# Kernel optimization log

Hardware: AMD Instinct MI355X
Metric: run time of the kernel (lower is better)

The kernel has to match this reference:

```python
import jax, jax.numpy as jnp
import numpy as np

D = 768
Y_DIM = 3
Z_DIM = 5
LN_EPS = 1e-5
COS_EPS = 1e-8  # F.cosine_similarity eps


def setup_inputs() -> dict:
    key = jax.random.key(0)
    ks = jax.random.split(key, 12)
    B, L = 64, 512
    s = 1.0 / np.sqrt(D)
    return {
        "embeddings": jax.random.normal(ks[0], (B, L, D), jnp.float32),
        "W1": jax.random.normal(ks[1], (D, D), jnp.float32) * s,
        "b1": jnp.zeros((D,), jnp.float32),
        "W2": jax.random.normal(ks[2], (D, D), jnp.float32) * s,
        "b2": jnp.zeros((D,), jnp.float32),
        "gamma": jnp.ones((D,), jnp.float32),
        "beta": jnp.zeros((D,), jnp.float32),
        "Wy": jax.random.normal(ks[3], (D, Y_DIM), jnp.float32) * s,
        "by": jnp.zeros((Y_DIM,), jnp.float32),
        "Wz": jax.random.normal(ks[4], (D, Z_DIM), jnp.float32) * s,
        "bz": jnp.zeros((Z_DIM,), jnp.float32),
    }


def _attention_cal(data):
    # data: [B, L, D]. Original: pairwise cosine similarity [B,L,L], sum over j, /L,
    # anti_sigmoid = 1/(1+exp(x)), softmax over L.
    # Algebraic rewrite: sum_j cos(x_i, x_j) = n_i . (sum_j n_j) with n = x/||x||.
    L = data.shape[1]
    norm = jnp.linalg.norm(data, axis=-1, keepdims=True)
    n = data / jnp.maximum(norm, COS_EPS)              # [B, L, D]
    s = n.sum(axis=1)                                  # [B, D]
    attention_weight = jnp.einsum("bld,bd->bl", n, s) / L  # [B, L]
    anti_sig = 1.0 / (1.0 + jnp.exp(attention_weight))
    return jax.nn.softmax(anti_sig, axis=-1)           # [B, L]


def reference(embeddings, W1, b1, W2, b2, gamma, beta, Wy, by, Wz, bz):
    h1 = embeddings @ W1 + b1
    h2 = jax.nn.relu(h1) @ W2 + b2
    x = embeddings + h2
    mean = x.mean(axis=-1, keepdims=True)
    var = x.var(axis=-1, keepdims=True)
    ff = gamma * (x - mean) * jax.lax.rsqrt(var + LN_EPS) + beta  # [B, L, D]
    out1 = ff @ Wy + by  # [B, L, Y_DIM]
    out2 = ff @ Wz + bz  # [B, L, Z_DIM]
    return (out1, out2, _attention_cal(ff))
```

## Files before the change

kernel.cpp:

```cpp
#include <hip/hip_runtime.h>
#include <hip/hip_bf16.h>
#include <math.h>

#define D_DIM 768
#define B_DIM 64
#define L_DIM 512
#define M_DIM (B_DIM * L_DIM)
#define YD 3
#define ZD 5
#define NCAT 16
#define LN_EPS 1e-5f
#define COS_EPS 1e-8f

typedef short short8v __attribute__((ext_vector_type(8)));
typedef float f32x4  __attribute__((ext_vector_type(4)));

__device__ __forceinline__ unsigned short f2bf(float f) {
    unsigned u = __builtin_bit_cast(unsigned, f);
    u = (u + 0x7fffu + ((u >> 16) & 1u)) >> 16;
    return (unsigned short)u;
}
__device__ __forceinline__ float bf2f(unsigned short h) {
    unsigned u = ((unsigned)h) << 16;
    return __builtin_bit_cast(float, u);
}
__device__ __forceinline__ void split2(float v, unsigned short& h, unsigned short& l) {
    h = f2bf(v);
    l = f2bf(v - bf2f(h));
}

__device__ __forceinline__ void gld16(const void* g, void* l) {
    __builtin_amdgcn_global_load_lds(
        (const __attribute__((address_space(1))) void*)g,
        (__attribute__((address_space(3))) void*)l, 16, 0, 0);
}

__global__ __launch_bounds__(256)
void tsplit_kernel(const float* __restrict__ W1, const float* __restrict__ W2,
                   unsigned short* __restrict__ t1hi, unsigned short* __restrict__ t1lo,
                   unsigned short* __restrict__ t2hi, unsigned short* __restrict__ t2lo)
{
    const float* W = blockIdx.z ? W2 : W1;
    unsigned short* thi = blockIdx.z ? t2hi : t1hi;
    unsigned short* tlo = blockIdx.z ? t2lo : t1lo;
    __shared__ float t[32][33];
    const int tx = threadIdx.x & 31, ty = threadIdx.x >> 5;
    const int n0 = blockIdx.x * 32, k0 = blockIdx.y * 32;
    #pragma unroll
    for (int j = 0; j < 4; ++j)
        t[ty + 8 * j][tx] = W[(size_t)(k0 + ty + 8 * j) * D_DIM + n0 + tx];
    __syncthreads();
    #pragma unroll
    for (int j = 0; j < 4; ++j) {
        const float v = t[tx][ty + 8 * j];
        unsigned short h, l; split2(v, h, l);
        const size_t o = (size_t)(n0 + ty + 8 * j) * D_DIM + k0 + tx;
        thi[o] = h; tlo[o] = l;
    }
}

template<int MODE>
__global__ __launch_bounds__(256, 2)
void gemm_mfma(const float* __restrict__ Af,
               const unsigned short* __restrict__ Ahi, const unsigned short* __restrict__ Alo,
               const unsigned short* __restrict__ Bhi, const unsigned short* __restrict__ Blo,
               const float* __restrict__ bias, const float* __restrict__ resid,
               unsigned short* __restrict__ out_hi, unsigned short* __restrict__ out_lo)
{
    __shared__ short8v As_hi[512], As_lo[512], Bs_hi[512], Bs_lo[512];

    const int lin = blockIdx.y * gridDim.x + blockIdx.x;
    const int cpx = (gridDim.x * gridDim.y) >> 3;
    const int lid = (lin & 7) * cpx + (lin >> 3);
    const int bx  = lid % 6;
    const int by  = lid / 6;

    const int tid  = threadIdx.x;
    const int w    = tid >> 6;
    const int lane = tid & 63;
    const int m0   = by * 128;
    const int n0   = bx * 128;
    const int wm   = (w >> 1) * 64;
    const int wn   = (w & 1) * 64;

    const int rr = lane >> 2;
    const int cc = lane & 3;
    const int r0 = w * 32 + rr;
    const int r1 = r0 + 16;
    const int sw0 = (cc ^ ((r0 >> 1) & 3)) * 16;
    const int sw1 = (cc ^ ((r1 >> 1) & 3)) * 16;
    const size_t boff0 = (size_t)(n0 + r0) * 1536 + sw0;
    const size_t boff1 = (size_t)(n0 + r1) * 1536 + sw1;
    const char* pBhi = (const char*)Bhi; const char* pBlo = (const char*)Blo;
    short8v* const dBh0 = Bs_hi + w * 128;      short8v* const dBh1 = dBh0 + 64;
    short8v* const dBl0 = Bs_lo + w * 128;      short8v* const dBl1 = dBl0 + 64;

    const size_t aoff0 = (size_t)(m0 + r0) * 1536 + sw0;
    const size_t aoff1 = (size_t)(m0 + r1) * 1536 + sw1;
    const char* pAhi = (const char*)Ahi; const char* pAlo = (const char*)Alo;
    short8v* const dAh0 = As_hi + w * 128;      short8v* const dAh1 = dAh0 + 64;
    short8v* const dAl0 = As_lo + w * 128;      short8v* const dAl1 = dAl0 + 64;

    const int ar  = tid >> 1;
    const int ak0 = (tid & 1) * 16;
    const int asw = (ar >> 1) & 3;
    const int sA0 = ar * 4 + (((tid & 1) * 2 + 0) ^ asw);
    const int sA1 = ar * 4 + (((tid & 1) * 2 + 1) ^ asw);
    const float* gA = (MODE == 0) ? (Af + (size_t)(m0 + ar) * D_DIM + ak0) : nullptr;

    const int lc = lane & 15;
    const int lk = lane >> 4;
    int ia[4], ib[4];
    #pragma unroll
    for (int m = 0; m < 4; ++m) { const int r = wm + m * 16 + lc; ia[m] = r * 4 + (lk ^ ((r >> 1) & 3)); }
    #pragma unroll
    for (int n = 0; n < 4; ++n) { const int r = wn + n * 16 + lc; ib[n] = r * 4 + (lk ^ ((r >> 1) & 3)); }

    f32x4 acc[4][4];
    #pragma unroll
    for (int m = 0; m < 4; ++m)
        #pragma unroll
        for (int n = 0; n < 4; ++n) acc[m][n] = (f32x4)(0.f);

    for (int t = 0; t < 24; ++t) {
        const int kk2 = t * 64;
        gld16(pBhi + boff0 + kk2, dBh0);
        gld16(pBhi + boff1 + kk2, dBh1);
        gld16(pBlo + boff0 + kk2, dBl0);
        gld16(pBlo + boff1 + kk2, dBl1);
        if (MODE == 0) {
            const int kk = t * 32;
            float tmp[16];
            #pragma unroll
            for (int q = 0; q < 4; ++q) {
                const float4 f = *reinterpret_cast<const float4*>(gA + kk + q * 4);
                tmp[q * 4 + 0] = f.x; tmp[q * 4 + 1] = f.y;
                tmp[q * 4 + 2] = f.z; tmp[q * 4 + 3] = f.w;
            }
            short8v h0, h1, l0, l1;
            #pragma unroll
            for (int e = 0; e < 8; ++e) {
                unsigned short h, l;
                split2(tmp[e], h, l);     h0[e] = (short)h; l0[e] = (short)l;
                split2(tmp[8 + e], h, l); h1[e] = (short)h; l1[e] = (short)l;
            }
            As_hi[sA0] = h0; As_hi[sA1] = h1;
            As_lo[sA0] = l0; As_lo[sA1] = l1;
        } else {
            gld16(pAhi + aoff0 + kk2, dAh0);
            gld16(pAhi + aoff1 + kk2, dAh1);
            gld16(pAlo + aoff0 + kk2, dAl0);
            gld16(pAlo + aoff1 + kk2, dAl1);
        }
        __syncthreads();

        short8v ah[4], al[4], bh[4], bl[4];
        #pragma unroll
        for (int m = 0; m < 4; ++m) { ah[m] = As_hi[ia[m]]; al[m] = As_lo[ia[m]]; }
        #pragma unroll
        for (int n = 0; n < 4; ++n) { bh[n] = Bs_hi[ib[n]]; bl[n] = Bs_lo[ib[n]]; }

        #pragma unroll
        for (int m = 0; m < 4; ++m)
            #pragma unroll
            for (int n = 0; n < 4; ++n) {
                acc[m][n] = __builtin_amdgcn_mfma_f32_16x16x32_bf16(ah[m], bh[n], acc[m][n], 0, 0, 0);
                acc[m][n] = __builtin_amdgcn_mfma_f32_16x16x32_bf16(ah[m], bl[n], acc[m][n], 0, 0, 0);
                acc[m][n] = __builtin_amdgcn_mfma_f32_16x16x32_bf16(al[m], bh[n], acc[m][n], 0, 0, 0);
            }
        __syncthreads();
    }

    const int erow = lane >> 4;
    #pragma unroll
    for (int m = 0; m < 4; ++m) {
        #pragma unroll
        for (int n = 0; n < 4; ++n) {
            const int gcol = n0 + wn + n * 16 + lc;
            const float bv = bias[gcol];
            const int grow0 = m0 + wm + m * 16 + erow * 4;
            #pragma unroll
            for (int r = 0; r < 4; ++r) {
                float v = acc[m][n][r] + bv;
                const size_t o = (size_t)(grow0 + r) * D_DIM + gcol;
                if (MODE == 0) {
                    v = fmaxf(v, 0.f);
                    unsigned short h, l; split2(v, h, l);
                    out_hi[o] = h; out_lo[o] = l;
                } else {
                    out_hi[o] = f2bf(v + resid[o]);
                }
            }
        }
    }
}

__global__ __launch_bounds__(256)
void ln_kernel(const unsigned short* __restrict__ xfb, const float* __restrict__ gamma,
               const float* __restrict__ beta, unsigned short* __restrict__ ffb,
               float* __restrict__ rnorm)
{
    const int wave = threadIdx.x >> 6;
    const int lane = threadIdx.x & 63;
    const int row  = blockIdx.x * 4 + wave;
    const unsigned short* xr = xfb + (size_t)row * D_DIM;
    unsigned short* fr = ffb + (size_t)row * D_DIM;

    float v[12];
    float sum = 0.f, sumsq = 0.f;
    #pragma unroll
    for (int j = 0; j < 3; ++j) {
        const ushort4 f = *reinterpret_cast<const ushort4*>(&xr[j * 256 + lane * 4]);
        v[j * 4 + 0] = bf2f(f.x); v[j * 4 + 1] = bf2f(f.y);
        v[j * 4 + 2] = bf2f(f.z); v[j * 4 + 3] = bf2f(f.w);
    }
    #pragma unroll
    for (int e = 0; e < 12; ++e) { sum += v[e]; sumsq = fmaf(v[e], v[e], sumsq); }
    #pragma unroll
    for (int m = 1; m < 64; m <<= 1) {
        sum   += __shfl_xor(sum, m);
        sumsq += __shfl_xor(sumsq, m);
    }
    const float mean = sum * (1.f / 768.f);
    const float var  = sumsq * (1.f / 768.f) - mean * mean;
    const float rstd = 1.f / sqrtf(var + LN_EPS);

    float nsq = 0.f;
    #pragma unroll
    for (int j = 0; j < 3; ++j) {
        const int c = j * 256 + lane * 4;
        const float4 g  = *reinterpret_cast<const float4*>(&gamma[c]);
        const float4 bt = *reinterpret_cast<const float4*>(&beta[c]);
        float4 o;
        o.x = fmaf(g.x * (v[j*4+0] - mean), rstd, bt.x);
        o.y = fmaf(g.y * (v[j*4+1] - mean), rstd, bt.y);
        o.z = fmaf(g.z * (v[j*4+2] - mean), rstd, bt.z);
        o.w = fmaf(g.w * (v[j*4+3] - mean), rstd, bt.w);
        nsq = fmaf(o.x, o.x, nsq); nsq = fmaf(o.y, o.y, nsq);
        nsq = fmaf(o.z, o.z, nsq); nsq = fmaf(o.w, o.w, nsq);
        ushort4 ob;
        ob.x = f2bf(o.x); ob.y = f2bf(o.y); ob.z = f2bf(o.z); ob.w = f2bf(o.w);
        *reinterpret_cast<ushort4*>(&fr[c]) = ob;
    }
    #pragma unroll
    for (int m = 1; m < 64; m <<= 1) nsq += __shfl_xor(nsq, m);
    if (lane == 0) rnorm[row] = 1.f / fmaxf(sqrtf(nsq), COS_EPS);
}

__global__ __launch_bounds__(256)
void colsum_kernel(const unsigned short* __restrict__ ffb, const float* __restrict__ rnorm,
                   float* __restrict__ s_part)
{
    const int c = blockIdx.x * 256 + threadIdx.x;
    const int q = blockIdx.y;
    const int b = blockIdx.z;
    const unsigned short* fb = ffb + (size_t)b * L_DIM * D_DIM;
    const float* rb = rnorm + b * L_DIM;
    float acc = 0.f;
    #pragma unroll 4
    for (int l = q * 128; l < q * 128 + 128; ++l)
        acc = fmaf(bf2f(fb[(size_t)l * D_DIM + c]), rb[l], acc);
    s_part[((size_t)b * 4 + q) * D_DIM + c] = acc;
}

__global__ __launch_bounds__(256)
void wcat_kernel(const float* __restrict__ Wy, const float* __restrict__ Wz,
                 const float* __restrict__ s_part, unsigned short* __restrict__ wcat)
{
    const int b = blockIdx.x;
    unsigned short* wb = wcat + (size_t)b * NCAT * D_DIM;
    const float* sp = s_part + (size_t)b * 4 * D_DIM;
    for (int k = threadIdx.x; k < D_DIM; k += 256) {
        #pragma unroll
        for (int y = 0; y < YD; ++y) wb[y * D_DIM + k] = f2bf(Wy[k * YD + y]);
        #pragma unroll
        for (int z = 0; z < ZD; ++z) wb[(YD + z) * D_DIM + k] = f2bf(Wz[k * ZD + z]);
        wb[8 * D_DIM + k] = f2bf(sp[k] + sp[D_DIM + k] + sp[2 * D_DIM + k] + sp[3 * D_DIM + k]);
        #pragma unroll
        for (int n = 9; n < NCAT; ++n) wb[n * D_DIM + k] = 0;
    }
}

__global__ __launch_bounds__(256)
void rowout_mfma(const unsigned short* __restrict__ ffb, const unsigned short* __restrict__ wcat,
                 const float* __restrict__ rnorm,
                 const float* __restrict__ by, const float* __restrict__ bz,
                 float* __restrict__ out1, float* __restrict__ out2,
                 float* __restrict__ aw)
{
    const int w    = threadIdx.x >> 6;
    const int lane = threadIdx.x & 63;
    const int rbase = blockIdx.x * 64 + w * 16;
    const int b     = blockIdx.x >> 3;
    const int idx  = lane & 15;
    const int ak   = (lane >> 4) * 8;

    const unsigned short* arow = ffb + (size_t)(rbase + idx) * D_DIM + ak;
    const unsigned short* brow = wcat + ((size_t)b * NCAT + idx) * D_DIM + ak;

    f32x4 acc = (f32x4)(0.f);
    #pragma unroll 4
    for (int t = 0; t < 24; ++t) {
        const short8v a  = *reinterpret_cast<const short8v*>(arow + t * 32);
        const short8v bb = *reinterpret_cast<const short8v*>(brow + t * 32);
        acc = __builtin_amdgcn_mfma_f32_16x16x32_bf16(a, bb, acc, 0, 0, 0);
    }

    const int erow = lane >> 4;
    #pragma unroll
    for (int r = 0; r < 4; ++r) {
        const int row = rbase + erow * 4 + r;
        const float v = acc[r];
        if (idx < YD) {
            out1[(size_t)row * YD + idx] = v + by[idx];
        } else if (idx < YD + ZD) {
            out2[(size_t)row * ZD + (idx - YD)] = v + bz[idx - YD];
        } else if (idx == 8) {
            const float a_ = v * rnorm[row] * (1.f / (float)L_DIM);
            aw[row] = 1.f / (1.f + expf(a_));
        }
    }
}

__global__ __launch_bounds__(512)
void softmax_kernel(const float* __restrict__ aw, float* __restrict__ attn)
{
    __shared__ float red[8];
    const int b = blockIdx.x;
    const int t = threadIdx.x;
    const int wave = t >> 6, lane = t & 63;
    const float v = aw[b * L_DIM + t];

    float mx = v;
    #pragma unroll
    for (int m = 1; m < 64; m <<= 1) mx = fmaxf(mx, __shfl_xor(mx, m));
    if (lane == 0) red[wave] = mx;
    __syncthreads();
    mx = red[0];
    #pragma unroll
    for (int w = 1; w < 8; ++w) mx = fmaxf(mx, red[w]);
    __syncthreads();

    const float e = expf(v - mx);
    float sm = e;
    #pragma unroll
    for (int m = 1; m < 64; m <<= 1) sm += __shfl_xor(sm, m);
    if (lane == 0) red[wave] = sm;
    __syncthreads();
    float tot = 0.f;
    #pragma unroll
    for (int w = 0; w < 8; ++w) tot += red[w];

    attn[b * L_DIM + t] = e / tot;
}

extern "C" void kernel_launch(void* const* d_in, const int* in_sizes, int n_in,
                              void* d_out, int out_size, void* d_ws, size_t ws_size,
                              hipStream_t stream)
{
    const float* emb   = (const float*)d_in[0];
    const float* W1    = (const float*)d_in[1];
    const float* b1    = (const float*)d_in[2];
    const float* W2    = (const float*)d_in[3];
    const float* b2    = (const float*)d_in[4];
    const float* gamma = (const float*)d_in[5];
    const float* beta  = (const float*)d_in[6];
    const float* Wy    = (const float*)d_in[7];
    const float* by    = (const float*)d_in[8];
    const float* Wz    = (const float*)d_in[9];
    const float* bz    = (const float*)d_in[10];

    float* out = (float*)d_out;
    char*  p   = (char*)d_ws;

    const size_t MD = (size_t)M_DIM * D_DIM;

    unsigned short* h1_hi = (unsigned short*)p;  p += MD * 2;
    unsigned short* h1_lo = (unsigned short*)p;  p += MD * 2;
    unsigned short* xfb   = (unsigned short*)p;  p += MD * 2;
    unsigned short* w1t_hi = (unsigned short*)p; p += (size_t)D_DIM * D_DIM * 2;
    unsigned short* w1t_lo = (unsigned short*)p; p += (size_t)D_DIM * D_DIM * 2;
    unsigned short* w2t_hi = (unsigned short*)p; p += (size_t)D_DIM * D_DIM * 2;
    unsigned short* w2t_lo = (unsigned short*)p; p += (size_t)D_DIM * D_DIM * 2;
    float* rnorm  = (float*)p;                   p += (size_t)M_DIM * 4;
    float* awb    = (float*)p;                   p += (size_t)M_DIM * 4;
    float* s_part = (float*)p;                   p += (size_t)B_DIM * 4 * D_DIM * 4;
    unsigned short* wcat = (unsigned short*)p;

    unsigned short* ffb = h1_hi;

    float* out1 = out;
    float* out2 = out + (size_t)M_DIM * YD;
    float* attn = out + (size_t)M_DIM * (YD + ZD);

    tsplit_kernel<<<dim3(24, 24, 2), 256, 0, stream>>>(W1, W2, w1t_hi, w1t_lo,
                                                       w2t_hi, w2t_lo);

    const dim3 gg(D_DIM / 128, M_DIM / 128);
    gemm_mfma<0><<<gg, 256, 0, stream>>>(emb, nullptr, nullptr, w1t_hi, w1t_lo,
                                         b1, nullptr, h1_hi, h1_lo);
    gemm_mfma<1><<<gg, 256, 0, stream>>>(nullptr, h1_hi, h1_lo, w2t_hi, w2t_lo,
                                         b2, emb, xfb, nullptr);

    ln_kernel<<<M_DIM / 4, 256, 0, stream>>>(xfb, gamma, beta, ffb, rnorm);
    colsum_kernel<<<dim3(3, 4, B_DIM), 256, 0, stream>>>(ffb, rnorm, s_part);
    wcat_kernel<<<B_DIM, 256, 0, stream>>>(Wy, Wz, s_part, wcat);
    rowout_mfma<<<M_DIM / 64, 256, 0, stream>>>(ffb, wcat, rnorm, by, bz,
                                                out1, out2, awb);
    softmax_kernel<<<B_DIM, 512, 0, stream>>>(awb, attn);
}
```

Measured before the change: 426.2 us.

## Switch GEMM operands to fp16 with activations single-precision and weights split

Replaces the three-MFMA bf16 hi/lo split scheme with fp16 operands. Activations (embeddings and h1) are stored as a single fp16 value, while weights keep a hi/lo fp16 split, so each tile needs two MFMAs instead of three. This also halves A-side memory traffic and LDS use, drops the h1 lo buffer, and raises the launch-bounds occupancy hint from 2 to 4. The cost is accuracy: activations lose low-order bits and fp16 range limits could overflow for large values.

Result: faster. 403.8 us (-5.3%).

```diff
diff --git a/kernel.cpp b/kernel.cpp
--- a/kernel.cpp
+++ b/kernel.cpp
@@ -13,6 +13,7 @@
 #define COS_EPS 1e-8f
 
 typedef short short8v __attribute__((ext_vector_type(8)));
+typedef _Float16 half8v __attribute__((ext_vector_type(8)));
 typedef float f32x4  __attribute__((ext_vector_type(4)));
 
 __device__ __forceinline__ unsigned short f2bf(float f) {
@@ -24,9 +25,16 @@
     unsigned u = ((unsigned)h) << 16;
     return __builtin_bit_cast(float, u);
 }
-__device__ __forceinline__ void split2(float v, unsigned short& h, unsigned short& l) {
-    h = f2bf(v);
-    l = f2bf(v - bf2f(h));
+__device__ __forceinline__ unsigned short f2h(float f) {
+    _Float16 h = (_Float16)f;
+    return __builtin_bit_cast(unsigned short, h);
+}
+__device__ __forceinline__ float h2f(unsigned short u) {
+    return (float)__builtin_bit_cast(_Float16, u);
+}
+__device__ __forceinline__ void splith(float v, unsigned short& h, unsigned short& l) {
+    h = f2h(v);
+    l = f2h(v - h2f(h));
 }
 
 __device__ __forceinline__ void gld16(const void* g, void* l) {
@@ -37,12 +45,12 @@
 
 __global__ __launch_bounds__(256)
 void tsplit_kernel(const float* __restrict__ W1, const float* __restrict__ W2,
-                   unsigned short* __restrict__ t1hi, unsigned short* __restrict__ t1lo,
-                   unsigned short* __restrict__ t2hi, unsigned short* __restrict__ t2lo)
+                   unsigned short* __restrict__ t1h, unsigned short* __restrict__ t1l,
+                   unsigned short* __restrict__ t2h, unsigned short* __restrict__ t2l)
 {
     const float* W = blockIdx.z ? W2 : W1;
-    unsigned short* thi = blockIdx.z ? t2hi : t1hi;
-    unsigned short* tlo = blockIdx.z ? t2lo : t1lo;
+    unsigned short* th = blockIdx.z ? t2h : t1h;
+    unsigned short* tl = blockIdx.z ? t2l : t1l;
     __shared__ float t[32][33];
     const int tx = threadIdx.x & 31, ty = threadIdx.x >> 5;
     const int n0 = blockIdx.x * 32, k0 = blockIdx.y * 32;
@@ -53,21 +61,21 @@
     #pragma unroll
     for (int j = 0; j < 4; ++j) {
         const float v = t[tx][ty + 8 * j];
-        unsigned short h, l; split2(v, h, l);
+        unsigned short h, l; splith(v, h, l);
         const size_t o = (size_t)(n0 + ty + 8 * j) * D_DIM + k0 + tx;
-        thi[o] = h; tlo[o] = l;
+        th[o] = h; tl[o] = l;
     }
 }
 
 template<int MODE>
-__global__ __launch_bounds__(256, 2)
+__global__ __launch_bounds__(256, 4)
 void gemm_mfma(const float* __restrict__ Af,
-               const unsigned short* __restrict__ Ahi, const unsigned short* __restrict__ Alo,
-               const unsigned short* __restrict__ Bhi, const unsigned short* __restrict__ Blo,
+               const unsigned short* __restrict__ Ah,
+               const unsigned short* __restrict__ Bh, const unsigned short* __restrict__ Bl,
                const float* __restrict__ bias, const float* __restrict__ resid,
-               unsigned short* __restrict__ out_hi, unsigned short* __restrict__ out_lo)
-{
-    __shared__ short8v As_hi[512], As_lo[512], Bs_hi[512], Bs_lo[512];
+               unsigned short* __restrict__ out_u16)
+{
+    __shared__ short8v As[512], Bs_h[512], Bs_l[512];
 
     const int lin = blockIdx.y * gridDim.x + blockIdx.x;
     const int cpx = (gridDim.x * gridDim.y) >> 3;
@@ -91,15 +99,14 @@
     const int sw1 = (cc ^ ((r1 >> 1) & 3)) * 16;
     const size_t boff0 = (size_t)(n0 + r0) * 1536 + sw0;
     const size_t boff1 = (size_t)(n0 + r1) * 1536 + sw1;
-    const char* pBhi = (const char*)Bhi; const char* pBlo = (const char*)Blo;
-    short8v* const dBh0 = Bs_hi + w * 128;      short8v* const dBh1 = dBh0 + 64;
-    short8v* const dBl0 = Bs_lo + w * 128;      short8v* const dBl1 = dBl0 + 64;
+    const char* pBh = (const char*)Bh; const char* pBl = (const char*)Bl;
+    short8v* const dBh0 = Bs_h + w * 128;      short8v* const dBh1 = dBh0 + 64;
+    short8v* const dBl0 = Bs_l + w * 128;      short8v* const dBl1 = dBl0 + 64;
 
     const size_t aoff0 = (size_t)(m0 + r0) * 1536 + sw0;
     const size_t aoff1 = (size_t)(m0 + r1) * 1536 + sw1;
-    const char* pAhi = (const char*)Ahi; const char* pAlo = (const char*)Alo;
-    short8v* const dAh0 = As_hi + w * 128;      short8v* const dAh1 = dAh0 + 64;
-    short8v* const dAl0 = As_lo + w * 128;      short8v* const dAl1 = dAl0 + 64;
+    const char* pAh = (const char*)Ah;
+    short8v* const dA0 = As + w * 128;         short8v* const dA1 = dA0 + 64;
 
     const int ar  = tid >> 1;
     const int ak0 = (tid & 1) * 16;
@@ -124,10 +131,10 @@
 
     for (int t = 0; t < 24; ++t) {
         const int kk2 = t * 64;
-        gld16(pBhi + boff0 + kk2, dBh0);
-        gld16(pBhi + boff1 + kk2, dBh1);
-        gld16(pBlo + boff0 + kk2, dBl0);
-        gld16(pBlo + boff1 + kk2, dBl1);
+        gld16(pBh + boff0 + kk2, dBh0);
+        gld16(pBh + boff1 + kk2, dBh1);
+        gld16(pBl + boff0 + kk2, dBl0);
+        gld16(pBl + boff1 + kk2, dBl1);
         if (MODE == 0) {
             const int kk = t * 32;
             float tmp[16];
@@ -137,36 +144,34 @@
                 tmp[q * 4 + 0] = f.x; tmp[q * 4 + 1] = f.y;
                 tmp[q * 4 + 2] = f.z; tmp[q * 4 + 3] = f.w;
             }
-            short8v h0, h1, l0, l1;
+            short8v h0, h1;
             #pragma unroll
             for (int e = 0; e < 8; ++e) {
-                unsigned short h, l;
-                split2(tmp[e], h, l);     h0[e] = (short)h; l0[e] = (short)l;
-                split2(tmp[8 + e], h, l); h1[e] = (short)h; l1[e] = (short)l;
+                h0[e] = (short)f2h(tmp[e]);
+                h1[e] = (short)f2h(tmp[8 + e]);
             }
-            As_hi[sA0] = h0; As_hi[sA1] = h1;
-            As_lo[sA0] = l0; As_lo[sA1] = l1;
+            As[sA0] = h0; As[sA1] = h1;
         } else {
-            gld16(pAhi + aoff0 + kk2, dAh0);
-            gld16(pAhi + aoff1 + kk2, dAh1);
-            gld16(pAlo + aoff0 + kk2, dAl0);
-            gld16(pAlo + aoff1 + kk2, dAl1);
+            gld16(pAh + aoff0 + kk2, dA0);
+            gld16(pAh + aoff1 + kk2, dA1);
         }
         __syncthreads();
 
-        short8v ah[4], al[4], bh[4], bl[4];
-        #pragma unroll
-        for (int m = 0; m < 4; ++m) { ah[m] = As_hi[ia[m]]; al[m] = As_lo[ia[m]]; }
-        #pragma unroll
-        for (int n = 0; n < 4; ++n) { bh[n] = Bs_hi[ib[n]]; bl[n] = Bs_lo[ib[n]]; }
+        half8v a[4], bh[4], bl[4];
+        #pragma unroll
+        for (int m = 0; m < 4; ++m) a[m] = __builtin_bit_cast(half8v, As[ia[m]]);
+        #pragma unroll
+        for (int n = 0; n < 4; ++n) {
+            bh[n] = __builtin_bit_cast(half8v, Bs_h[ib[n]]);
+            bl[n] = __builtin_bit_cast(half8v, Bs_l[ib[n]]);
+        }
 
         #pragma unroll
         for (int m = 0; m < 4; ++m)
             #pragma unroll
             for (int n = 0; n < 4; ++n) {
-                acc[m][n] = __builtin_amdgcn_mfma_f32_16x16x32_bf16(ah[m], bh[n], acc[m][n], 0, 0, 0);
-                acc[m][n] = __builtin_amdgcn_mfma_f32_16x16x32_bf16(ah[m], bl[n], acc[m][n], 0, 0, 0);
-                acc[m][n] = __builtin_amdgcn_mfma_f32_16x16x32_bf16(al[m], bh[n], acc[m][n], 0, 0, 0);
+                acc[m][n] = __builtin_amdgcn_mfma_f32_16x16x32_f16(a[m], bh[n], acc[m][n], 0, 0, 0);
+                acc[m][n] = __builtin_amdgcn_mfma_f32_16x16x32_f16(a[m], bl[n], acc[m][n], 0, 0, 0);
             }
         __syncthreads();
     }
@@ -184,11 +189,9 @@
                 float v = acc[m][n][r] + bv;
                 const size_t o = (size_t)(grow0 + r) * D_DIM + gcol;
                 if (MODE == 0) {
-                    v = fmaxf(v, 0.f);
-                    unsigned short h, l; split2(v, h, l);
-                    out_hi[o] = h; out_lo[o] = l;
+                    out_u16[o] = f2h(fmaxf(v, 0.f));
                 } else {
-                    out_hi[o] = f2bf(v + resid[o]);
+                    out_u16[o] = f2bf(v + resid[o]);
                 }
             }
         }
@@ -375,32 +378,31 @@
 
     const size_t MD = (size_t)M_DIM * D_DIM;
 
-    unsigned short* h1_hi = (unsigned short*)p;  p += MD * 2;
-    unsigned short* h1_lo = (unsigned short*)p;  p += MD * 2;
+    unsigned short* h1h   = (unsigned short*)p;  p += MD * 2;
     unsigned short* xfb   = (unsigned short*)p;  p += MD * 2;
-    unsigned short* w1t_hi = (unsigned short*)p; p += (size_t)D_DIM * D_DIM * 2;
-    unsigned short* w1t_lo = (unsigned short*)p; p += (size_t)D_DIM * D_DIM * 2;
-    unsigned short* w2t_hi = (unsigned short*)p; p += (size_t)D_DIM * D_DIM * 2;
-    unsigned short* w2t_lo = (unsigned short*)p; p += (size_t)D_DIM * D_DIM * 2;
+    unsigned short* w1t_h = (unsigned short*)p;  p += (size_t)D_DIM * D_DIM * 2;
+    unsigned short* w1t_l = (unsigned short*)p;  p += (size_t)D_DIM * D_DIM * 2;
+    unsigned short* w2t_h = (unsigned short*)p;  p += (size_t)D_DIM * D_DIM * 2;
+    unsigned short* w2t_l = (unsigned short*)p;  p += (size_t)D_DIM * D_DIM * 2;
     float* rnorm  = (float*)p;                   p += (size_t)M_DIM * 4;
     float* awb    = (float*)p;                   p += (size_t)M_DIM * 4;
     float* s_part = (float*)p;                   p += (size_t)B_DIM * 4 * D_DIM * 4;
     unsigned short* wcat = (unsigned short*)p;
 
-    unsigned short* ffb = h1_hi;
+    unsigned short* ffb = h1h;
 
     float* out1 = out;
     float* out2 = out + (size_t)M_DIM * YD;
     float* attn = out + (size_t)M_DIM * (YD + ZD);
 
-    tsplit_kernel<<<dim3(24, 24, 2), 256, 0, stream>>>(W1, W2, w1t_hi, w1t_lo,
-                                                       w2t_hi, w2t_lo);
+    tsplit_kernel<<<dim3(24, 24, 2), 256, 0, stream>>>(W1, W2, w1t_h, w1t_l,
+                                                       w2t_h, w2t_l);
 
     const dim3 gg(D_DIM / 128, M_DIM / 128);
-    gemm_mfma<0><<<gg, 256, 0, stream>>>(emb, nullptr, nullptr, w1t_hi, w1t_lo,
-                                         b1, nullptr, h1_hi, h1_lo);
-    gemm_mfma<1><<<gg, 256, 0, stream>>>(nullptr, h1_hi, h1_lo, w2t_hi, w2t_lo,
-                                         b2, emb, xfb, nullptr);
+    gemm_mfma<0><<<gg, 256, 0, stream>>>(emb, nullptr, w1t_h, w1t_l,
+                                         b1, nullptr, h1h);
+    gemm_mfma<1><<<gg, 256, 0, stream>>>(nullptr, h1h, w2t_h, w2t_l,
+                                         b2, emb, xfb);
 
     ln_kernel<<<M_DIM / 4, 256, 0, stream>>>(xfb, gamma, beta, ffb, rnorm);
     colsum_kernel<<<dim3(3, 4, B_DIM), 256, 0, stream>>>(ffb, rnorm, s_part);
```
